# Kernel tuning notes

Hardware: AMD Instinct MI355X
Metric: run time of the kernel (lower is better)

The kernel has to match this reference:

```python
import jax, jax.numpy as jnp
import numpy as np

N, E, F, H1, H2 = 8192, 131072, 512, 32, 16
POS_WEIGHT = 10.0


def gcn_conv(x, W, src, dst, n):
    h = x @ W  # [n, out]
    deg = jax.ops.segment_sum(jnp.ones(dst.shape[0], x.dtype), dst, num_segments=n) + 1.0  # self-loop
    dinv = jnp.where(deg > 0, deg ** -0.5, 0.0)
    coef = dinv[src] * dinv[dst]  # [E]
    out = jax.ops.segment_sum(h[src] * coef[:, None], dst, num_segments=n)
    out = out + h * (dinv * dinv)[:, None]  # self-loop message
    return out


def setup_inputs() -> dict:
    key = jax.random.key(0)
    ks = jax.random.split(key, 8)
    x = jax.random.normal(ks[0], (N, F), dtype=jnp.float32)
    edge_index = jax.random.randint(ks[1], (2, E), 0, N, dtype=jnp.int32)
    adj_label = jax.random.randint(ks[2], (N, N), 0, 2, dtype=jnp.int32)
    eps = jax.random.normal(ks[3], (N, H2), dtype=jnp.float32)
    norm = jnp.ones((1,), dtype=jnp.float32)
    W1 = jax.random.normal(ks[4], (F, H1), dtype=jnp.float32) * 0.05
    W2 = jax.random.normal(ks[5], (H1, H2), dtype=jnp.float32) * 0.05
    W3 = jax.random.normal(ks[6], (H1, H2), dtype=jnp.float32) * 0.05
    return {"x": x, "edge_index": edge_index, "adj_label": adj_label,
            "eps": eps, "norm": norm, "W1": W1, "W2": W2, "W3": W3}


def reference(x, edge_index, adj_label, eps, norm, W1, W2, W3):
    n = x.shape[0]
    src, dst = edge_index[0], edge_index[1]
    h1 = jax.nn.relu(gcn_conv(x, W1, src, dst, n))
    mu = gcn_conv(h1, W2, src, dst, n)
    logvar = gcn_conv(h1, W3, src, dst, n)
    # reparameterize: std = exp(logvar) (as in source, not exp(0.5*logvar))
    z = eps * jnp.exp(logvar) + mu
    logits = z @ z.T  # [N, N] inner-product decode
    y = adj_label.astype(logits.dtype)
    # BCEWithLogitsLoss with pos_weight, numerically stable
    sp = jax.nn.softplus(-logits)
    bce = jnp.mean(POS_WEIGHT * y * sp + (1.0 - y) * (logits + sp))
    cost = norm[0] * bce
    kld = (-0.5 / n) * jnp.mean(jnp.sum(1.0 + 2.0 * logvar - mu ** 2 - jnp.exp(logvar) ** 2, axis=1))
    return cost + kld, mu
```

## Files before the change

### kernel.cpp

```cpp
#include <hip/hip_runtime.h>
#include <cstdint>
#include <cstddef>

#define N_NODES 8192
#define N_EDGES 131072
#define F_IN    512
#define H1C     32
#define H2C     16


__device__ __forceinline__ float block_reduce_sum(float v, int nthreads) {
    #pragma unroll
    for (int off = 32; off; off >>= 1) v += __shfl_down(v, off, 64);
    __shared__ float sred[16];
    int lane = threadIdx.x & 63, wid = threadIdx.x >> 6;
    if (lane == 0) sred[wid] = v;
    __syncthreads();
    float s = 0.0f;
    if (threadIdx.x == 0) {
        int nw = nthreads >> 6;
        for (int i = 0; i < nw; ++i) s += sred[i];
    }
    return s;
}

__device__ __forceinline__ float bce_elem(float l, int y) {
    float lse = __logf(1.0f + __expf(-fabsf(l)));
    float sp  = lse + fmaxf(l, 0.0f);
    float w   = (float)y;
    return fmaf(sp, fmaf(9.0f, w, 1.0f), -10.0f * w * l);
}

__device__ __forceinline__ float rfl(float x) {
    return __int_as_float(__builtin_amdgcn_readfirstlane(__float_as_int(x)));
}


__global__ void k_init(float4* __restrict__ p) {
    int gid = blockIdx.x * 256 + threadIdx.x;
    float4 zz = {0.0f, 0.0f, 0.0f, 0.0f};
    p[gid] = zz;
}

__global__ void k_deg(const int* __restrict__ dst, int* __restrict__ deg) {
    int e = blockIdx.x * 256 + threadIdx.x;
    if (e < N_EDGES) atomicAdd(&deg[dst[e]], 1);
}

__global__ void k_scan(const int* __restrict__ deg, int* __restrict__ rowptr,
                       float* __restrict__ dinv) {
    int t = threadIdx.x;
    int base = t * 32;
    int vals[32];
    int s = 0;
    #pragma unroll
    for (int j = 0; j < 32; ++j) {
        vals[j] = deg[base + j];
        s += vals[j];
        dinv[base + j] = rsqrtf((float)(vals[j] + 1));
    }
    int lane = t & 63, wid = t >> 6;
    int inc = s;
    #pragma unroll
    for (int off = 1; off < 64; off <<= 1) {
        int n = __shfl_up(inc, off, 64);
        if (lane >= off) inc += n;
    }
    __shared__ int wsum[4];
    if (lane == 63) wsum[wid] = inc;
    __syncthreads();
    int woff = 0;
    for (int i = 0; i < wid; ++i) woff += wsum[i];
    int run = woff + inc - s;
    #pragma unroll
    for (int j = 0; j < 32; ++j) { rowptr[base + j] = run; run += vals[j]; }
    if (t == 255) rowptr[8192] = run;
}

__global__ void k_fill(const int* __restrict__ src, const int* __restrict__ dst,
                       const int* __restrict__ rowptr, const float* __restrict__ dinv,
                       int* __restrict__ cursor, int* __restrict__ csr_src,
                       float* __restrict__ csr_coef) {
    int e = blockIdx.x * 256 + threadIdx.x;
    int d = dst[e], sv = src[e];
    int slot = rowptr[d] + atomicAdd(&cursor[d], 1);
    csr_src[slot] = sv;
    csr_coef[slot] = dinv[sv];
}

__global__ void __launch_bounds__(256)
k_gemm1(const float* __restrict__ x, const float* __restrict__ W1,
        float* __restrict__ h) {
    __shared__ float wsm[F_IN][H1C];
    int tid = threadIdx.x;
    {
        float4* wd = (float4*)wsm;
        const float4* wsrc = (const float4*)W1;
        #pragma unroll
        for (int i = 0; i < 16; ++i) wd[tid + i * 256] = wsrc[tid + i * 256];
    }
    __syncthreads();

    int row = (blockIdx.x << 5) + (tid >> 3);
    int c4 = (tid & 7) << 2;
    const float4* xp = (const float4*)&x[(size_t)row * F_IN];

    float ax = 0.f, ay = 0.f, az = 0.f, aw = 0.f;
    #pragma unroll 8
    for (int k4 = 0; k4 < F_IN / 4; ++k4) {
        float4 xv = xp[k4];
        float4 w0 = *(const float4*)&wsm[k4 * 4 + 0][c4];
        float4 w1 = *(const float4*)&wsm[k4 * 4 + 1][c4];
        float4 w2 = *(const float4*)&wsm[k4 * 4 + 2][c4];
        float4 w3 = *(const float4*)&wsm[k4 * 4 + 3][c4];
        ax = fmaf(xv.x, w0.x, ax); ay = fmaf(xv.x, w0.y, ay);
        az = fmaf(xv.x, w0.z, az); aw = fmaf(xv.x, w0.w, aw);
        ax = fmaf(xv.y, w1.x, ax); ay = fmaf(xv.y, w1.y, ay);
        az = fmaf(xv.y, w1.z, az); aw = fmaf(xv.y, w1.w, aw);
        ax = fmaf(xv.z, w2.x, ax); ay = fmaf(xv.z, w2.y, ay);
        az = fmaf(xv.z, w2.z, az); aw = fmaf(xv.z, w2.w, aw);
        ax = fmaf(xv.w, w3.x, ax); ay = fmaf(xv.w, w3.y, ay);
        az = fmaf(xv.w, w3.z, az); aw = fmaf(xv.w, w3.w, aw);
    }
    float4 v; v.x = ax; v.y = ay; v.z = az; v.w = aw;
    *(float4*)&h[(size_t)row * H1C + c4] = v;
}

__global__ void __launch_bounds__(256)
k_gather1(const int* __restrict__ csr_src, const float* __restrict__ csr_coef,
          const int* __restrict__ rowptr, const float* __restrict__ h,
          const float* __restrict__ dinv, float* __restrict__ agg1) {
    int row = blockIdx.x * 4 + (threadIdx.x >> 6);
    int lane = threadIdx.x & 63;
    int f = lane & 31, half = lane >> 5;
    int beg = rowptr[row], end = rowptr[row + 1];
    float acc = 0.0f;
    for (int sl = beg + half; sl < end; sl += 2) {
        int s = csr_src[sl];
        float c = csr_coef[sl];
        acc = fmaf(h[(s << 5) + f], c, acc);
    }
    acc += __shfl_down(acc, 32, 64);
    if (half == 0)
        agg1[(row << 5) + f] = acc * dinv[row];
}

__global__ void k_gemm2(const float* __restrict__ agg1, const float* __restrict__ h,
                        const float* __restrict__ dinv, const float* __restrict__ W2,
                        const float* __restrict__ W3, float* __restrict__ h2mu,
                        float* __restrict__ h2lv) {
    __shared__ float h1s[8][33];
    __shared__ float w2s[H1C * H2C], w3s[H1C * H2C];
    int tid = threadIdx.x;
    int rb = blockIdx.x * 8;
    for (int i = tid; i < H1C * H2C; i += 256) { w2s[i] = W2[i]; w3s[i] = W3[i]; }
    {
        int r = tid >> 5, c = tid & 31;
        int row = rb + r;
        float di = dinv[row], d2 = di * di;
        h1s[r][c] = fmaxf(fmaf(h[(row << 5) + c], d2, agg1[(row << 5) + c]), 0.0f);
    }
    __syncthreads();
    int r = tid >> 5, cc = tid & 31, col = cc & 15;
    const float* wsrc = (cc & 16) ? w3s : w2s;
    float acc = 0.0f;
    #pragma unroll
    for (int k = 0; k < H1C; ++k) acc += h1s[r][k] * wsrc[(k << 4) + col];
    int row = rb + r;
    if (cc & 16) h2lv[(row << 4) + col] = acc;
    else         h2mu[(row << 4) + col] = acc;
}

__global__ void __launch_bounds__(256)
k_gather2(const int* __restrict__ csr_src, const float* __restrict__ csr_coef,
          const int* __restrict__ rowptr, const float* __restrict__ h2mu,
          const float* __restrict__ h2lv, const float* __restrict__ dinv,
          float* __restrict__ aggmu, float* __restrict__ agglv) {
    int row = blockIdx.x * 4 + (threadIdx.x >> 6);
    int lane = threadIdx.x & 63;
    int f = lane & 31, half = lane >> 5;
    int ff = f & 15;
    const float* hsrc = (f < 16) ? h2mu : h2lv;
    int beg = rowptr[row], end = rowptr[row + 1];
    float acc = 0.0f;
    for (int sl = beg + half; sl < end; sl += 2) {
        int s = csr_src[sl];
        float c = csr_coef[sl];
        acc = fmaf(hsrc[(s << 4) + ff], c, acc);
    }
    acc += __shfl_down(acc, 32, 64);
    if (half == 0) {
        float v = acc * dinv[row];
        if (f < 16) aggmu[(row << 4) + ff] = v;
        else        agglv[(row << 4) + ff] = v;
    }
}

__global__ void k_zmu(const float* __restrict__ aggmu, const float* __restrict__ agglv,
                      const float* __restrict__ h2mu, const float* __restrict__ h2lv,
                      const float* __restrict__ dinv, const float* __restrict__ eps,
                      float* __restrict__ zbuf, float* __restrict__ out,
                      float* __restrict__ kldp) {
    int gid = blockIdx.x * 256 + threadIdx.x;
    int row = gid >> 4;
    float di = dinv[row], d2 = di * di;
    float m  = fmaf(h2mu[gid], d2, aggmu[gid]);
    float lv = fmaf(h2lv[gid], d2, agglv[gid]);
    float el = __expf(lv);
    float zv = fmaf(eps[gid], el, m);
    zbuf[gid] = zv;
    out[1 + gid] = m;
    float kt = 1.0f + 2.0f * lv - m * m - el * el;
    float bs = block_reduce_sum(kt, 256);
    if (threadIdx.x == 0) kldp[blockIdx.x] = bs;
}

__global__ void __launch_bounds__(256)
k_bce(const float* __restrict__ z, const int* __restrict__ adj,
      float* __restrict__ part) {
    int tid = threadIdx.x;
    int band = blockIdx.x & 7;
    int rblk = blockIdx.x >> 3;
    int col0 = (band << 10) + (tid << 2);
    int row0 = rblk << 5;

    float zc[4][16];
    {
        const float4* zp = (const float4*)&z[(size_t)col0 * H2C];
        #pragma unroll
        for (int c = 0; c < 4; ++c)
            #pragma unroll
            for (int q = 0; q < 4; ++q) {
                float4 v = zp[c * 4 + q];
                zc[c][q * 4 + 0] = v.x; zc[c][q * 4 + 1] = v.y;
                zc[c][q * 4 + 2] = v.z; zc[c][q * 4 + 3] = v.w;
            }
    }

    float lsum = 0.0f;
    #pragma unroll
    for (int step = 0; step < 8; ++step) {
        int r0 = row0 + (step << 2);
        const int* ap = adj + (size_t)r0 * N_NODES + col0;
        int4 y0 = *(const int4*)(ap);
        int4 y1 = *(const int4*)(ap + N_NODES);
        int4 y2 = *(const int4*)(ap + 2 * N_NODES);
        int4 y3 = *(const int4*)(ap + 3 * N_NODES);

        float zr[4][16];
        {
            const float4* zp = (const float4*)&z[(size_t)r0 * H2C];
            #pragma unroll
            for (int q = 0; q < 16; ++q) {
                float4 v = zp[q];
                int r = q >> 2, qq = (q & 3) << 2;
                zr[r][qq + 0] = rfl(v.x); zr[r][qq + 1] = rfl(v.y);
                zr[r][qq + 2] = rfl(v.z); zr[r][qq + 3] = rfl(v.w);
            }
        }

        float a[4][4];
        #pragma unroll
        for (int r = 0; r < 4; ++r)
            #pragma unroll
            for (int c = 0; c < 4; ++c) a[r][c] = 0.0f;
        #pragma unroll
        for (int k = 0; k < 16; ++k) {
            #pragma unroll
            for (int r = 0; r < 4; ++r) {
                float zv = zr[r][k];
                a[r][0] = fmaf(zv, zc[0][k], a[r][0]);
                a[r][1] = fmaf(zv, zc[1][k], a[r][1]);
                a[r][2] = fmaf(zv, zc[2][k], a[r][2]);
                a[r][3] = fmaf(zv, zc[3][k], a[r][3]);
            }
        }
        lsum += bce_elem(a[0][0], y0.x) + bce_elem(a[0][1], y0.y)
              + bce_elem(a[0][2], y0.z) + bce_elem(a[0][3], y0.w);
        lsum += bce_elem(a[1][0], y1.x) + bce_elem(a[1][1], y1.y)
              + bce_elem(a[1][2], y1.z) + bce_elem(a[1][3], y1.w);
        lsum += bce_elem(a[2][0], y2.x) + bce_elem(a[2][1], y2.y)
              + bce_elem(a[2][2], y2.z) + bce_elem(a[2][3], y2.w);
        lsum += bce_elem(a[3][0], y3.x) + bce_elem(a[3][1], y3.y)
              + bce_elem(a[3][2], y3.z) + bce_elem(a[3][3], y3.w);
    }

    float bs = block_reduce_sum(lsum, 256);
    if (tid == 0) part[blockIdx.x] = bs;
}

__global__ void k_final(const float* __restrict__ part, const float* __restrict__ kldp,
                        const float* __restrict__ norm, float* __restrict__ out) {
    double s = 0.0, k = 0.0;
    for (int i = threadIdx.x; i < 2048; i += 256) s += (double)part[i];
    for (int i = threadIdx.x; i < 512; i += 256) k += (double)kldp[i];
    #pragma unroll
    for (int off = 32; off; off >>= 1) {
        s += __shfl_down(s, off, 64);
        k += __shfl_down(k, off, 64);
    }
    __shared__ double ss[4], kk[4];
    int lane = threadIdx.x & 63, wid = threadIdx.x >> 6;
    if (lane == 0) { ss[wid] = s; kk[wid] = k; }
    __syncthreads();
    if (threadIdx.x == 0) {
        double st = ss[0] + ss[1] + ss[2] + ss[3];
        double kt = kk[0] + kk[1] + kk[2] + kk[3];
        double bce = st / ((double)N_NODES * (double)N_NODES);
        double kld = (-0.5 / (double)N_NODES) * (kt / (double)N_NODES);
        out[0] = (float)((double)norm[0] * bce + kld);
    }
}


extern "C" void kernel_launch(void* const* d_in, const int* in_sizes, int n_in,
                              void* d_out, int out_size, void* d_ws, size_t ws_size,
                              hipStream_t stream) {
    const float* x    = (const float*)d_in[0];
    const int*   ei   = (const int*)d_in[1];
    const int*   adj  = (const int*)d_in[2];
    const float* eps  = (const float*)d_in[3];
    const float* norm = (const float*)d_in[4];
    const float* W1   = (const float*)d_in[5];
    const float* W2   = (const float*)d_in[6];
    const float* W3   = (const float*)d_in[7];
    float* out = (float*)d_out;
    char*  ws  = (char*)d_ws;

    const int* src = ei;
    const int* dst = ei + N_EDGES;

    int*   deg      = (int*)  (ws + 0);
    int*   cursor   = (int*)  (ws + 32768);
    int*   rowptr   = (int*)  (ws + 65536);
    float* dinv     = (float*)(ws + 102400);
    int*   csr_src  = (int*)  (ws + 135168);
    float* csr_coef = (float*)(ws + 659456);
    float* h        = (float*)(ws + 1183744);
    float* agg1     = (float*)(ws + 2232320);
    float* h2mu     = (float*)(ws + 3280896);
    float* h2lv     = (float*)(ws + 3805184);
    float* aggmu    = (float*)(ws + 4329472);
    float* agglv    = (float*)(ws + 4853760);
    float* zbuf     = (float*)(ws + 5378048);
    float* part     = (float*)(ws + 5902336);
    float* kldp     = (float*)(ws + 5910528);

    k_init<<<16, 256, 0, stream>>>((float4*)deg);
    k_deg<<<N_EDGES / 256, 256, 0, stream>>>(dst, deg);
    k_scan<<<1, 256, 0, stream>>>(deg, rowptr, dinv);
    k_fill<<<N_EDGES / 256, 256, 0, stream>>>(src, dst, rowptr, dinv, cursor, csr_src, csr_coef);
    k_gemm1<<<N_NODES / 32, 256, 0, stream>>>(x, W1, h);
    k_gather1<<<N_NODES / 4, 256, 0, stream>>>(csr_src, csr_coef, rowptr, h, dinv, agg1);
    k_gemm2<<<N_NODES / 8, 256, 0, stream>>>(agg1, h, dinv, W2, W3, h2mu, h2lv);
    k_gather2<<<N_NODES / 4, 256, 0, stream>>>(csr_src, csr_coef, rowptr, h2mu, h2lv, dinv, aggmu, agglv);
    k_zmu<<<(N_NODES * H2C) / 256, 256, 0, stream>>>(aggmu, agglv, h2mu, h2lv, dinv, eps, zbuf, out, kldp);
    k_bce<<<2048, 256, 0, stream>>>(zbuf, adj, part);
    k_final<<<1, 256, 0, stream>>>(part, kldp, norm, out);
}
```

Baseline: 146.3 us.

## Fuse GCN gathers with dense epilogues and retile BCE to two columns per thread

Merges the layer-1 gather with the ReLU and the W2/W3 projection into one kernel, and merges the layer-2 gather with the reparameterization, mu output and KLD partial sums into another. This removes two kernel launches and the intermediate agg1, aggmu and agglv buffers that each made a round trip through global memory. Separately, the BCE kernel now has each thread cover 2 columns instead of 4, using 4096 blocks instead of 2048, and the final reduction is resized to match. The narrower BCE tile raises parallelism but uses int2 loads of the adjacency matrix and reloads z rows twice as often, which could hurt its streaming bandwidth.

```diff
diff --git a/kernel.cpp b/kernel.cpp
--- a/kernel.cpp
+++ b/kernel.cpp
@@ -127,11 +127,23 @@
 }
 
 __global__ void __launch_bounds__(256)
-k_gather1(const int* __restrict__ csr_src, const float* __restrict__ csr_coef,
-          const int* __restrict__ rowptr, const float* __restrict__ h,
-          const float* __restrict__ dinv, float* __restrict__ agg1) {
-    int row = blockIdx.x * 4 + (threadIdx.x >> 6);
-    int lane = threadIdx.x & 63;
+k_g1g2(const int* __restrict__ csr_src, const float* __restrict__ csr_coef,
+       const int* __restrict__ rowptr, const float* __restrict__ h,
+       const float* __restrict__ dinv, const float* __restrict__ W2,
+       const float* __restrict__ W3, float* __restrict__ h2mu,
+       float* __restrict__ h2lv) {
+    __shared__ float w2s[H1C * H2C], w3s[H1C * H2C];
+    __shared__ float h1s[4][33];
+    int tid = threadIdx.x;
+    {
+        w2s[tid] = W2[tid]; w2s[tid + 256] = W2[tid + 256];
+        w3s[tid] = W3[tid]; w3s[tid + 256] = W3[tid + 256];
+    }
+    __syncthreads();
+
+    int w = tid >> 6;
+    int row = blockIdx.x * 4 + w;
+    int lane = tid & 63;
     int f = lane & 31, half = lane >> 5;
     int beg = rowptr[row], end = rowptr[row + 1];
     float acc = 0.0f;
@@ -141,43 +153,31 @@
         acc = fmaf(h[(s << 5) + f], c, acc);
     }
     acc += __shfl_down(acc, 32, 64);
-    if (half == 0)
-        agg1[(row << 5) + f] = acc * dinv[row];
-}
-
-__global__ void k_gemm2(const float* __restrict__ agg1, const float* __restrict__ h,
-                        const float* __restrict__ dinv, const float* __restrict__ W2,
-                        const float* __restrict__ W3, float* __restrict__ h2mu,
-                        float* __restrict__ h2lv) {
-    __shared__ float h1s[8][33];
-    __shared__ float w2s[H1C * H2C], w3s[H1C * H2C];
+    if (half == 0) {
+        float di = dinv[row], d2 = di * di;
+        float a1 = acc * di;
+        h1s[w][f] = fmaxf(fmaf(h[(row << 5) + f], d2, a1), 0.0f);
+    }
+    if (half == 0) {
+        const float* wsrc = (f < 16) ? w2s : w3s;
+        int col = f & 15;
+        float o = 0.0f;
+        #pragma unroll
+        for (int k = 0; k < H1C; ++k) o = fmaf(h1s[w][k], wsrc[(k << 4) + col], o);
+        if (f < 16) h2mu[(row << 4) + col] = o;
+        else        h2lv[(row << 4) + col] = o;
+    }
+}
+
+__global__ void __launch_bounds__(256)
+k_g2z(const int* __restrict__ csr_src, const float* __restrict__ csr_coef,
+      const int* __restrict__ rowptr, const float* __restrict__ h2mu,
+      const float* __restrict__ h2lv, const float* __restrict__ dinv,
+      const float* __restrict__ eps, float* __restrict__ zbuf,
+      float* __restrict__ out, float* __restrict__ kldp) {
     int tid = threadIdx.x;
-    int rb = blockIdx.x * 8;
-    for (int i = tid; i < H1C * H2C; i += 256) { w2s[i] = W2[i]; w3s[i] = W3[i]; }
-    {
-        int r = tid >> 5, c = tid & 31;
-        int row = rb + r;
-        float di = dinv[row], d2 = di * di;
-        h1s[r][c] = fmaxf(fmaf(h[(row << 5) + c], d2, agg1[(row << 5) + c]), 0.0f);
-    }
-    __syncthreads();
-    int r = tid >> 5, cc = tid & 31, col = cc & 15;
-    const float* wsrc = (cc & 16) ? w3s : w2s;
-    float acc = 0.0f;
-    #pragma unroll
-    for (int k = 0; k < H1C; ++k) acc += h1s[r][k] * wsrc[(k << 4) + col];
-    int row = rb + r;
-    if (cc & 16) h2lv[(row << 4) + col] = acc;
-    else         h2mu[(row << 4) + col] = acc;
-}
-
-__global__ void __launch_bounds__(256)
-k_gather2(const int* __restrict__ csr_src, const float* __restrict__ csr_coef,
-          const int* __restrict__ rowptr, const float* __restrict__ h2mu,
-          const float* __restrict__ h2lv, const float* __restrict__ dinv,
-          float* __restrict__ aggmu, float* __restrict__ agglv) {
-    int row = blockIdx.x * 4 + (threadIdx.x >> 6);
-    int lane = threadIdx.x & 63;
+    int row = blockIdx.x * 4 + (tid >> 6);
+    int lane = tid & 63;
     int f = lane & 31, half = lane >> 5;
     int ff = f & 15;
     const float* hsrc = (f < 16) ? h2mu : h2lv;
@@ -189,52 +189,41 @@
         acc = fmaf(hsrc[(s << 4) + ff], c, acc);
     }
     acc += __shfl_down(acc, 32, 64);
-    if (half == 0) {
-        float v = acc * dinv[row];
-        if (f < 16) aggmu[(row << 4) + ff] = v;
-        else        agglv[(row << 4) + ff] = v;
-    }
-}
-
-__global__ void k_zmu(const float* __restrict__ aggmu, const float* __restrict__ agglv,
-                      const float* __restrict__ h2mu, const float* __restrict__ h2lv,
-                      const float* __restrict__ dinv, const float* __restrict__ eps,
-                      float* __restrict__ zbuf, float* __restrict__ out,
-                      float* __restrict__ kldp) {
-    int gid = blockIdx.x * 256 + threadIdx.x;
-    int row = gid >> 4;
     float di = dinv[row], d2 = di * di;
-    float m  = fmaf(h2mu[gid], d2, aggmu[gid]);
-    float lv = fmaf(h2lv[gid], d2, agglv[gid]);
-    float el = __expf(lv);
-    float zv = fmaf(eps[gid], el, m);
-    zbuf[gid] = zv;
-    out[1 + gid] = m;
-    float kt = 1.0f + 2.0f * lv - m * m - el * el;
-    float bs = block_reduce_sum(kt, 256);
-    if (threadIdx.x == 0) kldp[blockIdx.x] = bs;
+    float val = fmaf(hsrc[(row << 4) + ff], d2, acc * di);
+    float other = __shfl_xor(val, 16, 64);
+    float kterm = 0.0f;
+    if (half == 0 && f < 16) {
+        float m = val, lv = other;
+        float el = __expf(lv);
+        float zv = fmaf(eps[(row << 4) + ff], el, m);
+        zbuf[(row << 4) + ff] = zv;
+        out[1 + (row << 4) + ff] = m;
+        kterm = 1.0f + 2.0f * lv - m * m - el * el;
+    }
+    float bs = block_reduce_sum(kterm, 256);
+    if (tid == 0) kldp[blockIdx.x] = bs;
 }
 
 __global__ void __launch_bounds__(256)
 k_bce(const float* __restrict__ z, const int* __restrict__ adj,
       float* __restrict__ part) {
     int tid = threadIdx.x;
-    int band = blockIdx.x & 7;
-    int rblk = blockIdx.x >> 3;
-    int col0 = (band << 10) + (tid << 2);
+    int band = blockIdx.x & 15;
+    int rblk = blockIdx.x >> 4;
+    int col0 = (band << 9) + (tid << 1);
     int row0 = rblk << 5;
 
-    float zc[4][16];
+    float zc[2][16];
     {
         const float4* zp = (const float4*)&z[(size_t)col0 * H2C];
         #pragma unroll
-        for (int c = 0; c < 4; ++c)
-            #pragma unroll
-            for (int q = 0; q < 4; ++q) {
-                float4 v = zp[c * 4 + q];
-                zc[c][q * 4 + 0] = v.x; zc[c][q * 4 + 1] = v.y;
-                zc[c][q * 4 + 2] = v.z; zc[c][q * 4 + 3] = v.w;
-            }
+        for (int q = 0; q < 8; ++q) {
+            float4 v = zp[q];
+            int c = q >> 2, qq = (q & 3) << 2;
+            zc[c][qq + 0] = v.x; zc[c][qq + 1] = v.y;
+            zc[c][qq + 2] = v.z; zc[c][qq + 3] = v.w;
+        }
     }
 
     float lsum = 0.0f;
@@ -242,10 +231,10 @@
     for (int step = 0; step < 8; ++step) {
         int r0 = row0 + (step << 2);
         const int* ap = adj + (size_t)r0 * N_NODES + col0;
-        int4 y0 = *(const int4*)(ap);
-        int4 y1 = *(const int4*)(ap + N_NODES);
-        int4 y2 = *(const int4*)(ap + 2 * N_NODES);
-        int4 y3 = *(const int4*)(ap + 3 * N_NODES);
+        int2 y0 = *(const int2*)(ap);
+        int2 y1 = *(const int2*)(ap + N_NODES);
+        int2 y2 = *(const int2*)(ap + 2 * N_NODES);
+        int2 y3 = *(const int2*)(ap + 3 * N_NODES);
 
         float zr[4][16];
         {
@@ -259,11 +248,9 @@
             }
         }
 
-        float a[4][4];
-        #pragma unroll
-        for (int r = 0; r < 4; ++r)
-            #pragma unroll
-            for (int c = 0; c < 4; ++c) a[r][c] = 0.0f;
+        float a[4][2];
+        #pragma unroll
+        for (int r = 0; r < 4; ++r) { a[r][0] = 0.0f; a[r][1] = 0.0f; }
         #pragma unroll
         for (int k = 0; k < 16; ++k) {
             #pragma unroll
@@ -271,18 +258,12 @@
                 float zv = zr[r][k];
                 a[r][0] = fmaf(zv, zc[0][k], a[r][0]);
                 a[r][1] = fmaf(zv, zc[1][k], a[r][1]);
-                a[r][2] = fmaf(zv, zc[2][k], a[r][2]);
-                a[r][3] = fmaf(zv, zc[3][k], a[r][3]);
             }
         }
-        lsum += bce_elem(a[0][0], y0.x) + bce_elem(a[0][1], y0.y)
-              + bce_elem(a[0][2], y0.z) + bce_elem(a[0][3], y0.w);
-        lsum += bce_elem(a[1][0], y1.x) + bce_elem(a[1][1], y1.y)
-              + bce_elem(a[1][2], y1.z) + bce_elem(a[1][3], y1.w);
-        lsum += bce_elem(a[2][0], y2.x) + bce_elem(a[2][1], y2.y)
-              + bce_elem(a[2][2], y2.z) + bce_elem(a[2][3], y2.w);
-        lsum += bce_elem(a[3][0], y3.x) + bce_elem(a[3][1], y3.y)
-              + bce_elem(a[3][2], y3.z) + bce_elem(a[3][3], y3.w);
+        lsum += bce_elem(a[0][0], y0.x) + bce_elem(a[0][1], y0.y);
+        lsum += bce_elem(a[1][0], y1.x) + bce_elem(a[1][1], y1.y);
+        lsum += bce_elem(a[2][0], y2.x) + bce_elem(a[2][1], y2.y);
+        lsum += bce_elem(a[3][0], y3.x) + bce_elem(a[3][1], y3.y);
     }
 
     float bs = block_reduce_sum(lsum, 256);
@@ -292,8 +273,8 @@
 __global__ void k_final(const float* __restrict__ part, const float* __restrict__ kldp,
                         const float* __restrict__ norm, float* __restrict__ out) {
     double s = 0.0, k = 0.0;
-    for (int i = threadIdx.x; i < 2048; i += 256) s += (double)part[i];
-    for (int i = threadIdx.x; i < 512; i += 256) k += (double)kldp[i];
+    for (int i = threadIdx.x; i < 4096; i += 256) s += (double)part[i];
+    for (int i = threadIdx.x; i < 2048; i += 256) k += (double)kldp[i];
     #pragma unroll
     for (int off = 32; off; off >>= 1) {
         s += __shfl_down(s, off, 64);
@@ -337,24 +318,19 @@
     int*   csr_src  = (int*)  (ws + 135168);
     float* csr_coef = (float*)(ws + 659456);
     float* h        = (float*)(ws + 1183744);
-    float* agg1     = (float*)(ws + 2232320);
     float* h2mu     = (float*)(ws + 3280896);
     float* h2lv     = (float*)(ws + 3805184);
-    float* aggmu    = (float*)(ws + 4329472);
-    float* agglv    = (float*)(ws + 4853760);
     float* zbuf     = (float*)(ws + 5378048);
     float* part     = (float*)(ws + 5902336);
-    float* kldp     = (float*)(ws + 5910528);
+    float* kldp     = (float*)(ws + 5918720);
 
     k_init<<<16, 256, 0, stream>>>((float4*)deg);
     k_deg<<<N_EDGES / 256, 256, 0, stream>>>(dst, deg);
     k_scan<<<1, 256, 0, stream>>>(deg, rowptr, dinv);
     k_fill<<<N_EDGES / 256, 256, 0, stream>>>(src, dst, rowptr, dinv, cursor, csr_src, csr_coef);
     k_gemm1<<<N_NODES / 32, 256, 0, stream>>>(x, W1, h);
-    k_gather1<<<N_NODES / 4, 256, 0, stream>>>(csr_src, csr_coef, rowptr, h, dinv, agg1);
-    k_gemm2<<<N_NODES / 8, 256, 0, stream>>>(agg1, h, dinv, W2, W3, h2mu, h2lv);
-    k_gather2<<<N_NODES / 4, 256, 0, stream>>>(csr_src, csr_coef, rowptr, h2mu, h2lv, dinv, aggmu, agglv);
-    k_zmu<<<(N_NODES * H2C) / 256, 256, 0, stream>>>(aggmu, agglv, h2mu, h2lv, dinv, eps, zbuf, out, kldp);
-    k_bce<<<2048, 256, 0, stream>>>(zbuf, adj, part);
+    k_g1g2<<<N_NODES / 4, 256, 0, stream>>>(csr_src, csr_coef, rowptr, h, dinv, W2, W3, h2mu, h2lv);
+    k_g2z<<<N_NODES / 4, 256, 0, stream>>>(csr_src, csr_coef, rowptr, h2mu, h2lv, dinv, eps, zbuf, out, kldp);
+    k_bce<<<4096, 256, 0, stream>>>(zbuf, adj, part);
     k_final<<<1, 256, 0, stream>>>(part, kldp, norm, out);
 }
```

Result: faster. 137.8 us (-5.8%).
